# Performance work log

Measured on AMD Instinct MI355X. Metric: run time of the kernel, lower is better.

The kernel has to match this reference:

```python
import jax, jax.numpy as jnp
import numpy as np

N_NODES = 100000


def _gcn_norm(edge_index, num_nodes):
    """Add self-loops and compute symmetric GCN normalization coefficients.
    Returns (src, dst, norm) for the augmented edge list."""
    loop = jnp.arange(num_nodes, dtype=edge_index.dtype)
    src = jnp.concatenate([edge_index[0], loop])
    dst = jnp.concatenate([edge_index[1], loop])
    deg = jax.ops.segment_sum(jnp.ones_like(src, dtype=jnp.float32), dst,
                              num_segments=num_nodes)
    dinv = jnp.where(deg > 0, jax.lax.rsqrt(deg), 0.0)
    norm = dinv[src] * dinv[dst]  # [E + N]
    return src, dst, norm


def setup_inputs() -> dict:
    key = jax.random.key(0)
    ks = jax.random.split(key, 7)
    d = 64
    E = 1000000
    x = jax.random.normal(ks[0], (N_NODES, d), dtype=jnp.float32)
    edge_index = jax.random.randint(ks[1], (2, E), 0, N_NODES, dtype=jnp.int64)
    s = 1.0 / np.sqrt(d)
    Ws = jax.random.normal(ks[2], (3, d, d), dtype=jnp.float32) * s
    bs = jax.random.normal(ks[3], (3, d), dtype=jnp.float32) * 0.02
    W_out = jax.random.normal(ks[4], (d, d), dtype=jnp.float32) * s
    b_out = jax.random.normal(ks[5], (d,), dtype=jnp.float32) * 0.02
    return {"x": x, "edge_index": edge_index, "Ws": Ws, "bs": bs,
            "W_out": W_out, "b_out": b_out}


def reference(x, edge_index, Ws, bs, W_out, b_out):
    num_nodes = x.shape[0]
    src, dst, norm = _gcn_norm(edge_index, num_nodes)  # fixed graph -> compute once
    for i in range(Ws.shape[0]):  # small fixed layer count
        h = x @ Ws[i]                              # [N, d] linear transform
        msg = norm[:, None] * h[src]               # gather + scale  [E+N, d]
        x = jax.ops.segment_sum(msg, dst, num_segments=num_nodes) + bs[i]
        x = jax.nn.relu(x)
    return x @ W_out + b_out
```

## Files before the change

kernel.cpp:

```cpp
#include <hip/hip_runtime.h>
#include <hip/hip_bf16.h>

#define D 64
#define BSHIFT 8
#define BNODES 256
#define BCAP 4096
#define PTILE 2048

typedef __attribute__((ext_vector_type(8))) short short8;
typedef __attribute__((ext_vector_type(4))) float float4v;


__device__ __forceinline__ float bf16u_to_f32(unsigned short u) {
  union { unsigned int i; float f; } c;
  c.i = ((unsigned int)u) << 16;
  return c.f;
}

__device__ __forceinline__ unsigned short f32_to_bf16u(float f) {
  union { float f; unsigned int u; } c;
  c.f = f;
  unsigned int r = (c.u + 0x7fffu + ((c.u >> 16) & 1u)) >> 16;
  return (unsigned short)r;
}


__global__ void k_probe(const void* W, const void* ei, int* flags) {
  int lane = threadIdx.x & 63;
  const unsigned short* wb = (const unsigned short*)W;
  bool big = false;
  for (int i = lane; i < 512; i += 64) {
    float v = bf16u_to_f32(wb[i]);
    if (!(fabsf(v) < 100.f)) big = true;
  }
  int anybig = __any(big);
  const int* e32 = (const int*)ei;
  bool nz = (e32[2 * lane + 1] != 0);
  int anynz = __any(nz);
  if (threadIdx.x == 0) {
    flags[0] = anybig ? 1 : 0;
    flags[1] = anynz ? 0 : 1;
  }
}


__global__ __launch_bounds__(256) void k_prep(
    const void* __restrict__ Ws, const void* __restrict__ Wout,
    const void* __restrict__ bs, const void* __restrict__ bout,
    const int* __restrict__ flags, unsigned short* __restrict__ WT,
    float* __restrict__ biasf, int* __restrict__ bucket_cursor) {
  int f32 = flags[0];
  int gid = blockIdx.x * 256 + threadIdx.x;
  int stride = gridDim.x * 256;

  for (int i = gid; i < 512; i += stride) bucket_cursor[i] = i * BCAP;

  for (int i = gid; i < 4 * 4096; i += stride) {
    int l = i >> 12;
    int r = i & 4095;
    int k = r >> 6;
    int nn = r & 63;
    unsigned short v;
    if (l < 3) {
      v = f32 ? f32_to_bf16u(((const float*)Ws)[l * 4096 + r])
              : ((const unsigned short*)Ws)[l * 4096 + r];
    } else {
      v = f32 ? f32_to_bf16u(((const float*)Wout)[r])
              : ((const unsigned short*)Wout)[r];
    }
    WT[l * 4096 + nn * 64 + k] = v;
  }
  for (int i = gid; i < 4 * 64; i += stride) {
    int l = i >> 6;
    int j = i & 63;
    float v;
    if (l < 3)
      v = f32 ? ((const float*)bs)[l * 64 + j]
              : bf16u_to_f32(((const unsigned short*)bs)[l * 64 + j]);
    else
      v = f32 ? ((const float*)bout)[j]
              : bf16u_to_f32(((const unsigned short*)bout)[j]);
    biasf[i] = v;
  }
}


__global__ __launch_bounds__(256) void k_partition(
    const void* __restrict__ ei, const int* __restrict__ flags,
    int* __restrict__ bucket_cursor, int* __restrict__ packed, int e) {
  __shared__ int lhist[512];
  __shared__ int lbase[512];
  int tid = threadIdx.x;
  int t0 = blockIdx.x * PTILE;
  int tend = min(t0 + PTILE, e);
  if (t0 >= e) return;
  int i64 = flags[1];

  for (int b = tid; b < 512; b += 256) lhist[b] = 0;
  __syncthreads();

  if (i64) {
    const long long* dst = (const long long*)ei + e;
    for (int i = t0 + tid; i < tend; i += 256)
      atomicAdd(&lhist[((int)dst[i]) >> BSHIFT], 1);
  } else {
    const int* dst = (const int*)ei + e;
    for (int i = t0 + tid; i < tend; i += 256)
      atomicAdd(&lhist[dst[i] >> BSHIFT], 1);
  }
  __syncthreads();

  for (int b = tid; b < 512; b += 256) {
    int c = lhist[b];
    lbase[b] = c ? atomicAdd(&bucket_cursor[b], c) : 0;
    lhist[b] = 0;
  }
  __syncthreads();

  if (i64) {
    const long long* srcp = (const long long*)ei;
    const long long* dstp = srcp + e;
    for (int i = t0 + tid; i < tend; i += 256) {
      int s = (int)srcp[i];
      int d = (int)dstp[i];
      int b = d >> BSHIFT;
      int r = atomicAdd(&lhist[b], 1);
      packed[lbase[b] + r] = (s << BSHIFT) | (d & (BNODES - 1));
    }
  } else {
    const int* srcp = (const int*)ei;
    const int* dstp = srcp + e;
    for (int i = t0 + tid; i < tend; i += 256) {
      int s = srcp[i];
      int d = dstp[i];
      int b = d >> BSHIFT;
      int r = atomicAdd(&lhist[b], 1);
      packed[lbase[b] + r] = (s << BSHIFT) | (d & (BNODES - 1));
    }
  }
}

__global__ __launch_bounds__(256) void k_sort_csr(
    const int* __restrict__ packed, const int* __restrict__ bucket_cursor,
    int* __restrict__ csr, int2* __restrict__ rowrange,
    float* __restrict__ dinv, int n) {
  __shared__ int lcnt[BNODES];
  __shared__ int lofs[BNODES];
  __shared__ int sbuf[BNODES];
  int tid = threadIdx.x;
  int bucket = blockIdx.x;
  int node0 = bucket << BSHIFT;
  int nodes = min(BNODES, n - node0);
  int s0 = bucket * BCAP;
  int s1 = bucket_cursor[bucket];
  lcnt[tid] = 0;
  __syncthreads();
  for (int i = s0 + tid; i < s1; i += 256)
    atomicAdd(&lcnt[packed[i] & (BNODES - 1)], 1);
  __syncthreads();
  int v = lcnt[tid];
  sbuf[tid] = v;
  __syncthreads();
  for (int off = 1; off < BNODES; off <<= 1) {
    int tv = (tid >= off) ? sbuf[tid - off] : 0;
    __syncthreads();
    sbuf[tid] += tv;
    __syncthreads();
  }
  int excl = sbuf[tid] - v;
  lofs[tid] = excl;
  lcnt[tid] = 0;
  if (tid < nodes) {
    rowrange[node0 + tid] = make_int2(s0 + excl, s0 + excl + v);
    dinv[node0 + tid] = rsqrtf((float)(v + 1));
  }
  __syncthreads();
  for (int i = s0 + tid; i < s1; i += 256) {
    int pk = packed[i];
    int ld = pk & (BNODES - 1);
    int r = atomicAdd(&lcnt[ld], 1);
    csr[s0 + lofs[ld] + r] = pk >> BSHIFT;
  }
}


__global__ __launch_bounds__(256) void k_scale(
    const void* __restrict__ x0, const int* __restrict__ flags,
    const float* __restrict__ dinv, ushort4* __restrict__ z, int n16) {
  int f32 = flags[0];
  int i = blockIdx.x * 256 + threadIdx.x;
  int stride = gridDim.x * 256;
  for (; i < n16; i += stride) {
    float d = dinv[i >> 4];
    ushort4 o;
    if (f32) {
      float4 v = ((const float4*)x0)[i];
      o.x = f32_to_bf16u(d * v.x);
      o.y = f32_to_bf16u(d * v.y);
      o.z = f32_to_bf16u(d * v.z);
      o.w = f32_to_bf16u(d * v.w);
    } else {
      ushort4 v = ((const ushort4*)x0)[i];
      o.x = f32_to_bf16u(d * bf16u_to_f32(v.x));
      o.y = f32_to_bf16u(d * bf16u_to_f32(v.y));
      o.z = f32_to_bf16u(d * bf16u_to_f32(v.z));
      o.w = f32_to_bf16u(d * bf16u_to_f32(v.w));
    }
    z[i] = o;
  }
}

__global__ __launch_bounds__(256, 4) void k_fused(
    const unsigned short* __restrict__ z, const int2* __restrict__ rowrange,
    const int* __restrict__ csr, const float* __restrict__ dinv,
    const unsigned short* __restrict__ WT, const float* __restrict__ biasf,
    unsigned short* __restrict__ out, int n, int scale_out) {
  __shared__ __align__(16) float part[4 * 2048];
  __shared__ unsigned short ybf[16 * 80];
  int tid = threadIdx.x;
  int lane = tid & 63;
  int w = tid >> 6;
  int q = lane >> 4;
  int f = lane & 15;
  int h = lane & 7;
  int g8 = lane >> 3;

  short8 b0 = *(const short8*)(WT + (size_t)(f + 16 * w) * 64 + q * 8);
  short8 b1 = *(const short8*)(WT + (size_t)(f + 16 * w) * 64 + 32 + q * 8);

  int row0 = blockIdx.x * 16;
  int base_node = row0 + w * 4;
  const short8* z8 = (const short8*)z;

  int rrw = 0;
  if (lane < 8) rrw = ((const int*)rowrange)[(size_t)base_node * 2 + lane];
  int rx0 = __shfl(rrw, 0, 64);
  int ry0 = __shfl(rrw, 1, 64);
  int rx1 = __shfl(rrw, 2, 64);
  int ry1 = __shfl(rrw, 3, 64);
  int rx2 = __shfl(rrw, 4, 64);
  int ry2 = __shfl(rrw, 5, 64);
  int rx3 = __shfl(rrw, 6, 64);
  int ry3 = __shfl(rrw, 7, 64);
  int deg0 = ry0 - rx0;
  int deg1 = ry1 - rx1;
  int deg2 = ry2 - rx2;
  int deg3 = ry3 - rx3;

  int jx = lane >> 4;
  int m = lane & 15;
  int rxj = (jx & 2) ? ((jx & 1) ? rx3 : rx2) : ((jx & 1) ? rx1 : rx0);
  int dgj = (jx & 2) ? ((jx & 1) ? deg3 : deg2) : ((jx & 1) ? deg1 : deg0);
  int coff = (m >= 1 && m <= dgj) ? (m - 1) : 0;
  int idx = csr[rxj + coff];
  if (m == 0) idx = base_node + jx;

  float a0[8] = {0, 0, 0, 0, 0, 0, 0, 0};
  float a1[8] = {0, 0, 0, 0, 0, 0, 0, 0};
  float a2[8] = {0, 0, 0, 0, 0, 0, 0, 0};
  float a3[8] = {0, 0, 0, 0, 0, 0, 0, 0};

  short8 g[8];
#pragma unroll
  for (int t = 0; t < 8; t++) {
    int u = ((t & 1) << 3) + g8;
    int sl = ((t >> 1) << 4) + u;
    int s = __shfl(idx, sl, 64);
    g[t] = z8[(size_t)s * 8 + h];
  }
#pragma unroll
  for (int t = 0; t < 8; t++) {
    int u = ((t & 1) << 3) + g8;
    const int j = t >> 1;
    int dg = (j == 0) ? deg0 : (j == 1) ? deg1 : (j == 2) ? deg2 : deg3;
    float vm = (u <= dg) ? 1.f : 0.f;
    float* aj = (j == 0) ? a0 : (j == 1) ? a1 : (j == 2) ? a2 : a3;
#pragma unroll
    for (int c = 0; c < 8; c++)
      aj[c] += vm * bf16u_to_f32((unsigned short)g[t][c]);
  }

#pragma unroll
  for (int j = 0; j < 4; j++) {
    int rx = (j == 0) ? rx0 : (j == 1) ? rx1 : (j == 2) ? rx2 : rx3;
    int dg = (j == 0) ? deg0 : (j == 1) ? deg1 : (j == 2) ? deg2 : deg3;
    float* aj = (j == 0) ? a0 : (j == 1) ? a1 : (j == 2) ? a2 : a3;
    for (int e0 = 15; e0 < dg; e0 += 8) {
      int e = e0 + g8;
      bool vv = e < dg;
      int s = csr[rx + (vv ? e : 0)];
      short8 tv = z8[(size_t)s * 8 + h];
      float vm = vv ? 1.f : 0.f;
#pragma unroll
      for (int c = 0; c < 8; c++)
        aj[c] += vm * bf16u_to_f32((unsigned short)tv[c]);
    }
  }

  char* pb = (char*)part + (w << 13);
  {
    int base_wg = g8 << 8;
#pragma unroll
    for (int j = 0; j < 4; j++) {
      const float* aj = (j == 0) ? a0 : (j == 1) ? a1 : (j == 2) ? a2 : a3;
      int jb = j << 11;
      *(float4*)(pb + jb + base_wg + ((((2 * h) ^ g8)) << 4)) =
          make_float4(aj[0], aj[1], aj[2], aj[3]);
      *(float4*)(pb + jb + base_wg + ((((2 * h + 1) ^ g8)) << 4)) =
          make_float4(aj[4], aj[5], aj[6], aj[7]);
    }
  }
  int jr = lane >> 4;
  int gr = lane & 15;
  float s0 = 0.f, s1 = 0.f, s2 = 0.f, s3 = 0.f;
#pragma unroll
  for (int gg = 0; gg < 8; gg++) {
    float4 v = *(const float4*)(pb + (jr << 11) + (gg << 8) + ((gr ^ gg) << 4));
    s0 += v.x;
    s1 += v.y;
    s2 += v.z;
    s3 += v.w;
  }
  {
    float dv = dinv[base_node + jr];
    unsigned int w0 = (unsigned int)f32_to_bf16u(dv * s0) |
                      ((unsigned int)f32_to_bf16u(dv * s1) << 16);
    unsigned int w1 = (unsigned int)f32_to_bf16u(dv * s2) |
                      ((unsigned int)f32_to_bf16u(dv * s3) << 16);
    *(uint2*)&ybf[(w * 4 + jr) * 80 + 4 * gr] = make_uint2(w0, w1);
  }
  __syncthreads();

  short8 fa0 = *(const short8*)&ybf[f * 80 + q * 8];
  short8 fa1 = *(const short8*)&ybf[f * 80 + 32 + q * 8];
  float4v zz = {0.f, 0.f, 0.f, 0.f};
  float4v acc = __builtin_amdgcn_mfma_f32_16x16x32_bf16(fa0, b0, zz, 0, 0, 0);
  acc = __builtin_amdgcn_mfma_f32_16x16x32_bf16(fa1, b1, acc, 0, 0, 0);

  float bv = biasf[16 * w + f];
  if (scale_out) {
    float4 dv4 = *(const float4*)(dinv + row0 + q * 4);
    float d[4] = {dv4.x, dv4.y, dv4.z, dv4.w};
#pragma unroll
    for (int reg = 0; reg < 4; reg++) {
      int row = row0 + q * 4 + reg;
      if (row < n)
        out[(size_t)row * 64 + 16 * w + f] =
            f32_to_bf16u(d[reg] * fmaxf(acc[reg] + bv, 0.f));
    }
  } else {
#pragma unroll
    for (int reg = 0; reg < 4; reg++) {
      int row = row0 + q * 4 + reg;
      if (row < n)
        out[(size_t)row * 64 + 16 * w + f] =
            f32_to_bf16u(fmaxf(acc[reg] + bv, 0.f));
    }
  }
}

__global__ __launch_bounds__(256) void k_gemm_final(
    const unsigned short* __restrict__ xin,
    const unsigned short* __restrict__ WT, const float* __restrict__ bias,
    void* __restrict__ out, const int* __restrict__ flags, int ntiles) {
  int lane = threadIdx.x & 63;
  int wid = threadIdx.x >> 6;
  int f = lane & 15;
  int q = lane >> 4;

  short8 bfr[4][2];
#pragma unroll
  for (int ct = 0; ct < 4; ct++)
#pragma unroll
    for (int kt = 0; kt < 2; kt++)
      bfr[ct][kt] =
          *(const short8*)(WT + (size_t)(f + 16 * ct) * 64 + kt * 32 + q * 8);

  int wave = blockIdx.x * 4 + wid;
  int nwaves = gridDim.x * 4;
  for (int t = wave; t < ntiles; t += nwaves) {
    int row0 = t * 16;
    const unsigned short* xr = xin + (size_t)(row0 + f) * 64 + q * 8;
    short8 a0 = *(const short8*)(xr);
    short8 a1 = *(const short8*)(xr + 32);
    float4v acc[4];
#pragma unroll
    for (int ct = 0; ct < 4; ct++) {
      float4v z = {0.f, 0.f, 0.f, 0.f};
      acc[ct] =
          __builtin_amdgcn_mfma_f32_16x16x32_bf16(a0, bfr[ct][0], z, 0, 0, 0);
      acc[ct] = __builtin_amdgcn_mfma_f32_16x16x32_bf16(a1, bfr[ct][1],
                                                        acc[ct], 0, 0, 0);
    }
    int f32o = flags[0];
    float bv[4];
#pragma unroll
    for (int ct = 0; ct < 4; ct++) bv[ct] = bias[f + 16 * ct];
    if (f32o) {
      float* op = (float*)out;
#pragma unroll
      for (int reg = 0; reg < 4; reg++) {
        size_t rb = (size_t)(row0 + q * 4 + reg) * 64 + f;
#pragma unroll
        for (int ct = 0; ct < 4; ct++) op[rb + 16 * ct] = acc[ct][reg] + bv[ct];
      }
    } else {
      unsigned short* op = (unsigned short*)out;
#pragma unroll
      for (int reg = 0; reg < 4; reg++) {
        size_t rb = (size_t)(row0 + q * 4 + reg) * 64 + f;
#pragma unroll
        for (int ct = 0; ct < 4; ct++)
          op[rb + 16 * ct] = f32_to_bf16u(acc[ct][reg] + bv[ct]);
      }
    }
  }
}


extern "C" void kernel_launch(void* const* d_in, const int* in_sizes, int n_in,
                              void* d_out, int out_size, void* d_ws,
                              size_t ws_size, hipStream_t stream) {
  const void* x0 = d_in[0];
  const void* ei = d_in[1];
  const void* Ws = d_in[2];
  const void* bs = d_in[3];
  const void* Wout = d_in[4];
  const void* bout = d_in[5];

  const int N = in_sizes[0] / D;
  const int E = in_sizes[1] / 2;
  const int NBUC = (N + BNODES - 1) >> BSHIFT;
  const int NT = (N + 15) / 16;

  char* p = (char*)d_ws;
  auto alloc = [&](size_t bytes) {
    char* r = p;
    p += (bytes + 511) & ~(size_t)511;
    return r;
  };
  int* flags = (int*)alloc(8);
  int* bucket_cursor = (int*)alloc(512 * 4);
  int* packed = (int*)alloc((size_t)512 * BCAP * 4);
  int* csr = (int*)alloc((size_t)512 * BCAP * 4);
  int2* rowrange = (int2*)alloc((size_t)N * 8);
  float* dinv = (float*)alloc((size_t)N * 4);
  unsigned short* WT = (unsigned short*)alloc(4 * 4096 * 2);
  float* biasf = (float*)alloc(4 * 64 * 4);
  unsigned short* za = (unsigned short*)alloc((size_t)N * D * 2);
  unsigned short* zb = (unsigned short*)alloc((size_t)N * D * 2);
  (void)ws_size;
  (void)n_in;
  (void)out_size;

  k_probe<<<1, 64, 0, stream>>>(Ws, ei, flags);
  k_prep<<<32, 256, 0, stream>>>(Ws, Wout, bs, bout, flags, WT, biasf,
                                 bucket_cursor);
  int ptiles = (E + PTILE - 1) / PTILE;
  k_partition<<<ptiles, 256, 0, stream>>>(ei, flags, bucket_cursor, packed, E);
  k_sort_csr<<<NBUC, 256, 0, stream>>>(packed, bucket_cursor, csr, rowrange,
                                       dinv, N);
  k_scale<<<1024, 256, 0, stream>>>(x0, flags, dinv, (ushort4*)za, N * 16);

  k_fused<<<NT, 256, 0, stream>>>(za, rowrange, csr, dinv, WT + 0 * 4096,
                                  biasf + 0 * 64, zb, N, 1);
  k_fused<<<NT, 256, 0, stream>>>(zb, rowrange, csr, dinv, WT + 1 * 4096,
                                  biasf + 1 * 64, za, N, 1);
  k_fused<<<NT, 256, 0, stream>>>(za, rowrange, csr, dinv, WT + 2 * 4096,
                                  biasf + 2 * 64, zb, N, 0);
  k_gemm_final<<<(NT + 3) / 4, 256, 0, stream>>>(zb, WT + 3 * 4096,
                                                 biasf + 3 * 64, d_out, flags,
                                                 NT);
}
```

Measured before the change: 228.1 us.

## Fuse probe and scale into other kernels, skip empty gathers, pack stores

Drops the standalone probe kernel; each kernel now computes the dtype flags inline with a wave vote. Merges the input scaling into the CSR sort kernel using dinv values held in shared memory, removing one launch and a dinv reload. In the fused aggregation kernel, the second gather half is skipped when a node has fewer than 8 neighbours, and output stores are packed as 32-bit pairs via a lane shuffle. It also doubles the partition tile size and hoists the bias loads in the final GEMM. The cost is redundant flag computation in every wave, plus more work and a fixed per-bucket schedule for the scale step inside the sort kernel.

```diff
diff --git a/kernel.cpp b/kernel.cpp
--- a/kernel.cpp
+++ b/kernel.cpp
@@ -5,11 +5,10 @@
 #define BSHIFT 8
 #define BNODES 256
 #define BCAP 4096
-#define PTILE 2048
+#define PTILE 4096
 
 typedef __attribute__((ext_vector_type(8))) short short8;
 typedef __attribute__((ext_vector_type(4))) float float4v;
-
 
 __device__ __forceinline__ float bf16u_to_f32(unsigned short u) {
   union { unsigned int i; float f; } c;
@@ -24,32 +23,30 @@
   return (unsigned short)r;
 }
 
-
-__global__ void k_probe(const void* W, const void* ei, int* flags) {
+__device__ __forceinline__ int wave_f32flag(const void* W) {
+  const unsigned short* wb = (const unsigned short*)W;
   int lane = threadIdx.x & 63;
-  const unsigned short* wb = (const unsigned short*)W;
   bool big = false;
   for (int i = lane; i < 512; i += 64) {
     float v = bf16u_to_f32(wb[i]);
     if (!(fabsf(v) < 100.f)) big = true;
   }
-  int anybig = __any(big);
+  return __any(big) ? 1 : 0;
+}
+__device__ __forceinline__ int wave_i64flag(const void* ei) {
   const int* e32 = (const int*)ei;
+  int lane = threadIdx.x & 63;
   bool nz = (e32[2 * lane + 1] != 0);
-  int anynz = __any(nz);
-  if (threadIdx.x == 0) {
-    flags[0] = anybig ? 1 : 0;
-    flags[1] = anynz ? 0 : 1;
-  }
+  return __any(nz) ? 0 : 1;
 }
 
 
 __global__ __launch_bounds__(256) void k_prep(
     const void* __restrict__ Ws, const void* __restrict__ Wout,
     const void* __restrict__ bs, const void* __restrict__ bout,
-    const int* __restrict__ flags, unsigned short* __restrict__ WT,
-    float* __restrict__ biasf, int* __restrict__ bucket_cursor) {
-  int f32 = flags[0];
+    unsigned short* __restrict__ WT, float* __restrict__ biasf,
+    int* __restrict__ bucket_cursor) {
+  int f32 = wave_f32flag(Ws);
   int gid = blockIdx.x * 256 + threadIdx.x;
   int stride = gridDim.x * 256;
 
@@ -86,15 +83,15 @@
 
 
 __global__ __launch_bounds__(256) void k_partition(
-    const void* __restrict__ ei, const int* __restrict__ flags,
-    int* __restrict__ bucket_cursor, int* __restrict__ packed, int e) {
+    const void* __restrict__ ei, int* __restrict__ bucket_cursor,
+    int* __restrict__ packed, int e) {
   __shared__ int lhist[512];
   __shared__ int lbase[512];
   int tid = threadIdx.x;
   int t0 = blockIdx.x * PTILE;
   int tend = min(t0 + PTILE, e);
   if (t0 >= e) return;
-  int i64 = flags[1];
+  int i64 = wave_i64flag(ei);
 
   for (int b = tid; b < 512; b += 256) lhist[b] = 0;
   __syncthreads();
@@ -143,10 +140,12 @@
 __global__ __launch_bounds__(256) void k_sort_csr(
     const int* __restrict__ packed, const int* __restrict__ bucket_cursor,
     int* __restrict__ csr, int2* __restrict__ rowrange,
-    float* __restrict__ dinv, int n) {
+    float* __restrict__ dinv, const void* __restrict__ x0,
+    const void* __restrict__ Ws, ushort4* __restrict__ za, int n) {
   __shared__ int lcnt[BNODES];
   __shared__ int lofs[BNODES];
   __shared__ int sbuf[BNODES];
+  __shared__ float sdinv[BNODES];
   int tid = threadIdx.x;
   int bucket = blockIdx.x;
   int node0 = bucket << BSHIFT;
@@ -170,9 +169,11 @@
   int excl = sbuf[tid] - v;
   lofs[tid] = excl;
   lcnt[tid] = 0;
+  float dvv = rsqrtf((float)(v + 1));
+  sdinv[tid] = dvv;
   if (tid < nodes) {
     rowrange[node0 + tid] = make_int2(s0 + excl, s0 + excl + v);
-    dinv[node0 + tid] = rsqrtf((float)(v + 1));
+    dinv[node0 + tid] = dvv;
   }
   __syncthreads();
   for (int i = s0 + tid; i < s1; i += 256) {
@@ -181,32 +182,29 @@
     int r = atomicAdd(&lcnt[ld], 1);
     csr[s0 + lofs[ld] + r] = pk >> BSHIFT;
   }
-}
-
-
-__global__ __launch_bounds__(256) void k_scale(
-    const void* __restrict__ x0, const int* __restrict__ flags,
-    const float* __restrict__ dinv, ushort4* __restrict__ z, int n16) {
-  int f32 = flags[0];
-  int i = blockIdx.x * 256 + threadIdx.x;
-  int stride = gridDim.x * 256;
-  for (; i < n16; i += stride) {
-    float d = dinv[i >> 4];
+
+  int f32 = wave_f32flag(Ws);
+  int total = nodes * 16;
+  for (int i = tid; i < total; i += 256) {
+    int r = i >> 4;
+    int c4 = i & 15;
+    float dv = sdinv[r];
+    size_t gi = (size_t)(node0 + r) * 16 + c4;
     ushort4 o;
     if (f32) {
-      float4 v = ((const float4*)x0)[i];
-      o.x = f32_to_bf16u(d * v.x);
-      o.y = f32_to_bf16u(d * v.y);
-      o.z = f32_to_bf16u(d * v.z);
-      o.w = f32_to_bf16u(d * v.w);
+      float4 vv = ((const float4*)x0)[gi];
+      o.x = f32_to_bf16u(dv * vv.x);
+      o.y = f32_to_bf16u(dv * vv.y);
+      o.z = f32_to_bf16u(dv * vv.z);
+      o.w = f32_to_bf16u(dv * vv.w);
     } else {
-      ushort4 v = ((const ushort4*)x0)[i];
-      o.x = f32_to_bf16u(d * bf16u_to_f32(v.x));
-      o.y = f32_to_bf16u(d * bf16u_to_f32(v.y));
-      o.z = f32_to_bf16u(d * bf16u_to_f32(v.z));
-      o.w = f32_to_bf16u(d * bf16u_to_f32(v.w));
-    }
-    z[i] = o;
+      ushort4 vv = ((const ushort4*)x0)[gi];
+      o.x = f32_to_bf16u(dv * bf16u_to_f32(vv.x));
+      o.y = f32_to_bf16u(dv * bf16u_to_f32(vv.y));
+      o.z = f32_to_bf16u(dv * bf16u_to_f32(vv.z));
+      o.w = f32_to_bf16u(dv * bf16u_to_f32(vv.w));
+    }
+    za[gi] = o;
   }
 }
 
@@ -263,16 +261,22 @@
   short8 g[8];
 #pragma unroll
   for (int t = 0; t < 8; t++) {
-    int u = ((t & 1) << 3) + g8;
-    int sl = ((t >> 1) << 4) + u;
+    const int j = t >> 1;
+    const int hi = t & 1;
+    int dg = (j == 0) ? deg0 : (j == 1) ? deg1 : (j == 2) ? deg2 : deg3;
+    if (hi && dg < 8) continue;
+    int u = (hi << 3) + g8;
+    int sl = (j << 4) + u;
     int s = __shfl(idx, sl, 64);
     g[t] = z8[(size_t)s * 8 + h];
   }
 #pragma unroll
   for (int t = 0; t < 8; t++) {
-    int u = ((t & 1) << 3) + g8;
     const int j = t >> 1;
+    const int hi = t & 1;
     int dg = (j == 0) ? deg0 : (j == 1) ? deg1 : (j == 2) ? deg2 : deg3;
+    if (hi && dg < 8) continue;
+    int u = (hi << 3) + g8;
     float vm = (u <= dg) ? 1.f : 0.f;
     float* aj = (j == 0) ? a0 : (j == 1) ? a1 : (j == 2) ? a2 : a3;
 #pragma unroll
@@ -338,23 +342,19 @@
   acc = __builtin_amdgcn_mfma_f32_16x16x32_bf16(fa1, b1, acc, 0, 0, 0);
 
   float bv = biasf[16 * w + f];
+  float dvr[4] = {1.f, 1.f, 1.f, 1.f};
   if (scale_out) {
     float4 dv4 = *(const float4*)(dinv + row0 + q * 4);
-    float d[4] = {dv4.x, dv4.y, dv4.z, dv4.w};
-#pragma unroll
-    for (int reg = 0; reg < 4; reg++) {
-      int row = row0 + q * 4 + reg;
-      if (row < n)
-        out[(size_t)row * 64 + 16 * w + f] =
-            f32_to_bf16u(d[reg] * fmaxf(acc[reg] + bv, 0.f));
-    }
-  } else {
-#pragma unroll
-    for (int reg = 0; reg < 4; reg++) {
-      int row = row0 + q * 4 + reg;
-      if (row < n)
-        out[(size_t)row * 64 + 16 * w + f] =
-            f32_to_bf16u(fmaxf(acc[reg] + bv, 0.f));
+    dvr[0] = dv4.x; dvr[1] = dv4.y; dvr[2] = dv4.z; dvr[3] = dv4.w;
+  }
+#pragma unroll
+  for (int reg = 0; reg < 4; reg++) {
+    int row = row0 + q * 4 + reg;
+    float val = dvr[reg] * fmaxf(acc[reg] + bv, 0.f);
+    unsigned int r16 = f32_to_bf16u(val);
+    unsigned int pr = (unsigned int)__shfl_xor((int)r16, 1, 64);
+    if (!(f & 1) && row < n) {
+      *(unsigned int*)&out[(size_t)row * 64 + 16 * w + f] = r16 | (pr << 16);
     }
   }
 }
@@ -362,11 +362,12 @@
 __global__ __launch_bounds__(256) void k_gemm_final(
     const unsigned short* __restrict__ xin,
     const unsigned short* __restrict__ WT, const float* __restrict__ bias,
-    void* __restrict__ out, const int* __restrict__ flags, int ntiles) {
+    void* __restrict__ out, const void* __restrict__ Ws, int ntiles) {
   int lane = threadIdx.x & 63;
   int wid = threadIdx.x >> 6;
   int f = lane & 15;
   int q = lane >> 4;
+  int f32o = wave_f32flag(Ws);
 
   short8 bfr[4][2];
 #pragma unroll
@@ -375,6 +376,10 @@
     for (int kt = 0; kt < 2; kt++)
       bfr[ct][kt] =
           *(const short8*)(WT + (size_t)(f + 16 * ct) * 64 + kt * 32 + q * 8);
+
+  float bv[4];
+#pragma unroll
+  for (int ct = 0; ct < 4; ct++) bv[ct] = bias[f + 16 * ct];
 
   int wave = blockIdx.x * 4 + wid;
   int nwaves = gridDim.x * 4;
@@ -392,10 +397,6 @@
       acc[ct] = __builtin_amdgcn_mfma_f32_16x16x32_bf16(a1, bfr[ct][1],
                                                         acc[ct], 0, 0, 0);
     }
-    int f32o = flags[0];
-    float bv[4];
-#pragma unroll
-    for (int ct = 0; ct < 4; ct++) bv[ct] = bias[f + 16 * ct];
     if (f32o) {
       float* op = (float*)out;
 #pragma unroll
@@ -439,7 +440,6 @@
     p += (bytes + 511) & ~(size_t)511;
     return r;
   };
-  int* flags = (int*)alloc(8);
   int* bucket_cursor = (int*)alloc(512 * 4);
   int* packed = (int*)alloc((size_t)512 * BCAP * 4);
   int* csr = (int*)alloc((size_t)512 * BCAP * 4);
@@ -453,14 +453,11 @@
   (void)n_in;
   (void)out_size;
 
-  k_probe<<<1, 64, 0, stream>>>(Ws, ei, flags);
-  k_prep<<<32, 256, 0, stream>>>(Ws, Wout, bs, bout, flags, WT, biasf,
-                                 bucket_cursor);
+  k_prep<<<32, 256, 0, stream>>>(Ws, Wout, bs, bout, WT, biasf, bucket_cursor);
   int ptiles = (E + PTILE - 1) / PTILE;
-  k_partition<<<ptiles, 256, 0, stream>>>(ei, flags, bucket_cursor, packed, E);
+  k_partition<<<ptiles, 256, 0, stream>>>(ei, bucket_cursor, packed, E);
   k_sort_csr<<<NBUC, 256, 0, stream>>>(packed, bucket_cursor, csr, rowrange,
-                                       dinv, N);
-  k_scale<<<1024, 256, 0, stream>>>(x0, flags, dinv, (ushort4*)za, N * 16);
+                                       dinv, x0, Ws, (ushort4*)za, N);
 
   k_fused<<<NT, 256, 0, stream>>>(za, rowrange, csr, dinv, WT + 0 * 4096,
                                   biasf + 0 * 64, zb, N, 1);
@@ -469,6 +466,6 @@
   k_fused<<<NT, 256, 0, stream>>>(za, rowrange, csr, dinv, WT + 2 * 4096,
                                   biasf + 2 * 64, zb, N, 0);
   k_gemm_final<<<(NT + 3) / 4, 256, 0, stream>>>(zb, WT + 3 * 4096,
-                                                 biasf + 3 * 64, d_out, flags,
+                                                 biasf + 3 * 64, d_out, Ws,
                                                  NT);
 }
```

New measurement: 236.5 us. 3.7% more time.
